# Kernel optimization log

Hardware: AMD Instinct MI355X
Metric: run time of the kernel (lower is better)

## Reference

```python
import jax, jax.numpy as jnp
import numpy as np

EPS = 1e-5  # torch BatchNorm2d default eps


def _conv(x, w, pad=0, groups=1):
    # x: NCHW, w: OIHW (torch layout); matches nn.Conv2d with given padding/groups
    return jax.lax.conv_general_dilated(
        x, w, window_strides=(1, 1), padding=[(pad, pad), (pad, pad)],
        dimension_numbers=("NCHW", "OIHW", "NCHW"), feature_group_count=groups)


def _bn_train(x, gamma, beta):
    # BatchNorm2d in training mode: batch stats over (N,H,W), biased variance
    m = jnp.mean(x, axis=(0, 2, 3), keepdims=True)
    v = jnp.mean(jnp.square(x - m), axis=(0, 2, 3), keepdims=True)
    return (x - m) * jax.lax.rsqrt(v + EPS) * gamma.reshape(1, -1, 1, 1) + beta.reshape(1, -1, 1, 1)


def setup_inputs() -> dict:
    key = jax.random.key(0)
    ks = jax.random.split(key, 8)
    B, C, H, W = 8, 32, 128, 128
    D = 8                      # num_directions
    WC = C * D                 # wavelet_channels = 256
    MID = WC * 2               # 512
    x = jax.random.normal(ks[0], (B, C, H, W), jnp.float32)
    # grouped directional filter bank: Conv2d(C, C*D, k=5, groups=C, bias=False)
    w_dir = jax.random.normal(ks[1], (WC, 1, 5, 5), jnp.float32) / np.sqrt(25.0)
    # wavelet_conv: Conv(WC->MID,3) BN ReLU Conv(MID->WC,3) BN ReLU
    w1 = jax.random.normal(ks[2], (MID, WC, 3, 3), jnp.float32) / np.sqrt(WC * 9.0)
    b1 = jnp.zeros((MID,), jnp.float32)
    g1 = jnp.ones((MID,), jnp.float32)
    be1 = jnp.zeros((MID,), jnp.float32)
    w2 = jax.random.normal(ks[3], (WC, MID, 3, 3), jnp.float32) / np.sqrt(MID * 9.0)
    b2 = jnp.zeros((WC,), jnp.float32)
    g2 = jnp.ones((WC,), jnp.float32)
    be2 = jnp.zeros((WC,), jnp.float32)
    # inverse_conv: Conv2d(WC, C, 1)
    w_inv = jax.random.normal(ks[4], (C, WC, 1, 1), jnp.float32) / np.sqrt(float(WC))
    b_inv = jnp.zeros((C,), jnp.float32)
    return {"x": x, "w_dir": w_dir, "w1": w1, "b1": b1, "g1": g1, "be1": be1,
            "w2": w2, "b2": b2, "g2": g2, "be2": be2, "w_inv": w_inv, "b_inv": b_inv}


def reference(x, w_dir, w1, b1, g1, be1, w2, b2, g2, be2, w_inv, b_inv):
    C = x.shape[1]
    # directional wavelet: grouped conv C -> C*8, k=5, pad=2, no bias
    coeffs = _conv(x, w_dir, pad=2, groups=C)                      # (B, 8C, H, W)
    # wavelet-domain conv stack
    h = _conv(coeffs, w1, pad=1) + b1.reshape(1, -1, 1, 1)         # (B, 16C, H, W)
    h = jax.nn.relu(_bn_train(h, g1, be1))
    h = _conv(h, w2, pad=1) + b2.reshape(1, -1, 1, 1)              # (B, 8C, H, W)
    h = jax.nn.relu(_bn_train(h, g2, be2))
    # inverse 1x1 conv back to C channels
    return _conv(h, w_inv) + b_inv.reshape(1, -1, 1, 1)            # (B, C, H, W)
```

## Files before the change

kernel.cpp:

```cpp
#include <hip/hip_runtime.h>

typedef unsigned short u16;
typedef unsigned int   u32;
typedef __attribute__((ext_vector_type(8)))  __bf16 bf16x8;
typedef __attribute__((ext_vector_type(4)))  float  f32x4;
typedef __attribute__((ext_vector_type(16))) float  f32x16;

__device__ __forceinline__ float bf2f(u16 u) {
    union { u32 i; float f; } v; v.i = ((u32)u) << 16; return v.f;
}
__device__ __forceinline__ u16 f2bf(float f) {
    u32 u = __float_as_uint(f);
    u32 r = (u + 0x7FFFu + ((u >> 16) & 1u)) >> 16;
    return (u16)r;
}

__device__ __forceinline__ void gl16(const u16* g, u16* l) {
    __builtin_amdgcn_global_load_lds(
        (const __attribute__((address_space(1))) unsigned int*)g,
        (__attribute__((address_space(3))) unsigned int*)l, 16, 0, 0);
}

__global__ __launch_bounds__(256) void dir_conv_k(const float* __restrict__ x,
                                                  const float* __restrict__ wd,
                                                  u16* __restrict__ coeffs) {
    int bid = blockIdx.x;
    int cc = bid & 3, y = (bid >> 2) & 127, n = bid >> 9;
    __shared__ float lx[5280];
    __shared__ float lw[1600];
    int t = threadIdx.x;
    for (int i = t; i < 1600; i += 256) {
        int ol = i / 25, tap = i - ol * 25;
        lw[tap * 64 + ol] = wd[(cc * 64 + ol) * 25 + tap];
    }
    for (int i = t; i < 5280; i += 256) {
        int c = i / 660, rem = i - c * 660;
        int ky = rem / 132, xx = rem - ky * 132;
        int gy = y - 2 + ky, gx = xx - 2;
        float v = 0.f;
        if (gy >= 0 && gy < 128 && gx >= 0 && gx < 128)
            v = x[(((n * 32 + cc * 8 + c) * 128 + gy) << 7) + gx];
        lx[i] = v;
    }
    __syncthreads();
    int px = t >> 1, oh = t & 1;
    float acc[4][8];
#pragma unroll
    for (int j = 0; j < 4; ++j)
#pragma unroll
        for (int d = 0; d < 8; ++d) acc[j][d] = 0.f;
#pragma unroll
    for (int j = 0; j < 4; ++j) {
        int cl = oh * 4 + j;
        const float* lxc = &lx[cl * 660];
#pragma unroll
        for (int ky = 0; ky < 5; ++ky)
#pragma unroll
            for (int kx = 0; kx < 5; ++kx) {
                float xv = lxc[ky * 132 + px + kx];
                const float* w8 = &lw[(ky * 5 + kx) * 64 + cl * 8];
#pragma unroll
                for (int d = 0; d < 8; ++d) acc[j][d] += xv * w8[d];
            }
    }
    long base = ((long)((n * 128 + y) * 128 + px)) * 256 + cc * 64 + oh * 32;
#pragma unroll
    for (int j = 0; j < 4; ++j) {
        uint4 o;
        o.x = (u32)f2bf(acc[j][0]) | ((u32)f2bf(acc[j][1]) << 16);
        o.y = (u32)f2bf(acc[j][2]) | ((u32)f2bf(acc[j][3]) << 16);
        o.z = (u32)f2bf(acc[j][4]) | ((u32)f2bf(acc[j][5]) << 16);
        o.w = (u32)f2bf(acc[j][6]) | ((u32)f2bf(acc[j][7]) << 16);
        *(uint4*)(coeffs + base + j * 8) = o;
    }
}

__global__ __launch_bounds__(256) void repack_w_k(const float* __restrict__ w,
                                                  u16* __restrict__ wp,
                                                  int OC, int IC, int total) {
    int f = blockIdx.x * 256 + threadIdx.x;
    if (f >= total) return;
    int KC = IC >> 5;
    int j  = f & 7;
    int h  = (f >> 3) & 1;
    int g  = f >> 4;
    int oc = g % OC; g /= OC;
    int s  = g & 1;  g >>= 1;
    int kc = g % KC;
    int tap = g / KC;
    int ic = kc * 32 + s * 16 + h * 8 + j;
    wp[f] = f2bf(w[(oc * IC + ic) * 9 + tap]);
}

#define KCITER(KCV, OFF)                                                       \
    {                                                                          \
        const int kc_ = (KCV);                                                 \
        const u16* lAu = (kc_ & 1) ? lA1 : lA0;                                \
        u16*       lAn = (kc_ & 1) ? lA0 : lA1;                                \
        __syncthreads();                                                       \
        {                                                                      \
            int au = ((h * 3) * W + lm) * 8;                                   \
            Ar[0][0] = *(const bf16x8*)(lAu + au);                             \
            Ar[0][1] = *(const bf16x8*)(lAu + au + 256);                       \
            Ar[0][2] = *(const bf16x8*)(lAu + au + 512);                       \
            Ar[0][3] = *(const bf16x8*)(lAu + au + 768);                       \
        }                                                                      \
        if (kc_ + 1 < KC) stage(lAn, kc_ + 1);                                 \
        _Pragma("unroll")                                                      \
        for (int i = 0; i < 18; ++i) {                                         \
            const int j   = (i + 1) % 18;                 \
            const int j3  = (i + 3) % 18;                \
            const int j3kc = (i >= 15) ? ((kc_ + 1 < KC) ? kc_ + 1 : 0) : kc_; \
            if (i != 17) {                                                     \
                const int jdy = j / 6, jdx = (j % 6) >> 1, js = j & 1;         \
                int au = (((js * 2 + h) * 3 + jdy) * W + jdx + lm) * 8;        \
                Ar[j & 1][0] = *(const bf16x8*)(lAu + au);                     \
                Ar[j & 1][1] = *(const bf16x8*)(lAu + au + 256);               \
                Ar[j & 1][2] = *(const bf16x8*)(lAu + au + 512);               \
                Ar[j & 1][3] = *(const bf16x8*)(lAu + au + 768);               \
            }                                                                  \
            bload(Br[(i + 3 + (OFF)) & 3], j3, j3kc);                          \
            __builtin_amdgcn_s_setprio(1);                                     \
            acc[0][0] = __builtin_amdgcn_mfma_f32_32x32x16_bf16(Ar[i & 1][0], Br[(i + (OFF)) & 3][0], acc[0][0], 0, 0, 0); \
            acc[0][1] = __builtin_amdgcn_mfma_f32_32x32x16_bf16(Ar[i & 1][0], Br[(i + (OFF)) & 3][1], acc[0][1], 0, 0, 0); \
            acc[1][0] = __builtin_amdgcn_mfma_f32_32x32x16_bf16(Ar[i & 1][1], Br[(i + (OFF)) & 3][0], acc[1][0], 0, 0, 0); \
            acc[1][1] = __builtin_amdgcn_mfma_f32_32x32x16_bf16(Ar[i & 1][1], Br[(i + (OFF)) & 3][1], acc[1][1], 0, 0, 0); \
            acc[2][0] = __builtin_amdgcn_mfma_f32_32x32x16_bf16(Ar[i & 1][2], Br[(i + (OFF)) & 3][0], acc[2][0], 0, 0, 0); \
            acc[2][1] = __builtin_amdgcn_mfma_f32_32x32x16_bf16(Ar[i & 1][2], Br[(i + (OFF)) & 3][1], acc[2][1], 0, 0, 0); \
            acc[3][0] = __builtin_amdgcn_mfma_f32_32x32x16_bf16(Ar[i & 1][3], Br[(i + (OFF)) & 3][0], acc[3][0], 0, 0, 0); \
            acc[3][1] = __builtin_amdgcn_mfma_f32_32x32x16_bf16(Ar[i & 1][3], Br[(i + (OFF)) & 3][1], acc[3][1], 0, 0, 0); \
            __builtin_amdgcn_s_setprio(0);                                     \
        }                                                                      \
    }

template<int IC, int OC>
__global__ __launch_bounds__(256, 2) void conv3_k(const u16* __restrict__ base,
                                                  u32 in_off,
                                                  const u16* __restrict__ wp,
                                                  const float* __restrict__ bias,
                                                  u32 zp_off,
                                                  u16* __restrict__ outp,
                                                  float* __restrict__ statp) {
    constexpr int KC = IC / 32;
    constexpr int W  = 130;
    constexpr int TU = 12 * W;
    constexpr int NFULL = TU / 256;
    constexpr int REM   = TU % 256;
    __shared__ u16 lA0[TU * 8];
    __shared__ u16 lA1[TU * 8];

    int bx0 = blockIdx.x;
    int bx = ((bx0 & 7) << 7) + (bx0 >> 3);
    int y = bx & 127, n = bx >> 7;
    int ocb = blockIdx.y;
    int t = threadIdx.x, lane = t & 63, wv = t >> 6;
    int lm = lane & 31, h = lane >> 5;
    int ocw = ocb * 256 + wv * 64;

    u32 off[NFULL + 1];
#pragma unroll
    for (int i = 0; i <= NFULL; ++i) {
        int u = (i == NFULL) ? (NFULL * 256 + lane) : (i * 256 + t);
        int icq = u / (3 * W);
        int r2  = u - icq * (3 * W);
        int dy  = r2 / W;
        int xx  = r2 - dy * W;
        int gy = y - 1 + dy, gx = xx - 1;
        bool ok = ((unsigned)gy < 128u) && ((unsigned)gx < 128u);
        off[i] = ok ? (in_off + (u32)((n * 128 + gy) * 128 + gx) * IC + (icq & 3) * 8)
                    : zp_off;
    }

    auto stage = [&](u16* dst, int kc) {
#pragma unroll
        for (int i = 0; i < NFULL; ++i)
            gl16(base + off[i] + kc * 32, dst + (i * 256 + wv * 64) * 8);
        if (wv == 0 && lane < REM)
            gl16(base + off[NFULL] + kc * 32, dst + NFULL * 256 * 8);
    };

    u32 wboff = (u32)(ocw + lm) * 16 + h * 8;
    bf16x8 Ar[2][4];
    bf16x8 Br[4][2];

    auto bload = [&](bf16x8* dst, int j, int kcv) {
        int jdy = j / 6, jdx = (j % 6) >> 1, js = j & 1;
        const u16* wb = wp + wboff
            + (u32)(((jdy * 3 + jdx) * KC + kcv) * 2 + js) * (OC * 16);
        dst[0] = *(const bf16x8*)wb;
        dst[1] = *(const bf16x8*)(wb + 512);
    };

    bload(Br[0], 0, 0);
    bload(Br[1], 1, 0);
    bload(Br[2], 2, 0);

    f32x16 acc[4][2];
#pragma unroll
    for (int mf = 0; mf < 4; ++mf)
#pragma unroll
        for (int nf = 0; nf < 2; ++nf)
#pragma unroll
            for (int r = 0; r < 16; ++r) acc[mf][nf][r] = 0.f;

    stage(lA0, 0);
    for (int kcb = 0; kcb < KC; kcb += 2) {
        KCITER(kcb, 0);
        KCITER(kcb + 1, 2);
    }

    long rowb = (long)(n * 128 + y) * 128;
    float ss[2] = {0.f, 0.f}, qq[2] = {0.f, 0.f};
#pragma unroll
    for (int nf = 0; nf < 2; ++nf) {
        int oc = ocw + nf * 32 + lm;
        float bi = bias[oc];
#pragma unroll
        for (int mf = 0; mf < 4; ++mf)
#pragma unroll
            for (int r = 0; r < 16; ++r) {
                int px = mf * 32 + (r & 3) + ((r >> 2) << 3) + (h << 2);
                u16 bv = f2bf(acc[mf][nf][r] + bi);
                outp[(rowb + px) * OC + oc] = bv;
                float vr = bf2f(bv);
                ss[nf] += vr;
                qq[nf] += vr * vr;
            }
    }
#pragma unroll
    for (int nf = 0; nf < 2; ++nf) {
        ss[nf] += __shfl_xor(ss[nf], 32);
        qq[nf] += __shfl_xor(qq[nf], 32);
    }
    if (h == 0) {
#pragma unroll
        for (int nf = 0; nf < 2; ++nf) {
            int oc = ocw + nf * 32 + lm;
            atomicAdd(&statp[oc * 2],     ss[nf]);
            atomicAdd(&statp[oc * 2 + 1], qq[nf]);
        }
    }
}

template<int C>
__global__ __launch_bounds__(256) void stats2_k(const float* __restrict__ part,
                                                const float* __restrict__ g,
                                                const float* __restrict__ be,
                                                float* __restrict__ ab) {
    int ch = blockIdx.x * 256 + threadIdx.x;
    if (ch >= C) return;
    float s = part[ch * 2], q = part[ch * 2 + 1];
    const float M = 131072.f;
    float mean = s / M;
    float var = q / M - mean * mean;
    float a = g[ch] * rsqrtf(var + 1e-5f);
    ab[ch * 2]     = a;
    ab[ch * 2 + 1] = be[ch] - mean * a;
}

__global__ __launch_bounds__(256) void bn_relu_k(u16* __restrict__ h,
                                                 const float* __restrict__ ab) {
    long idx8 = (long)blockIdx.x * 256 + threadIdx.x;
    u16* p = h + idx8 * 8;
    uint4 v = *(const uint4*)p;
    int chb = ((int)idx8 & 63) << 3;
    u32 w[4] = {v.x, v.y, v.z, v.w};
    u32 o[4];
#pragma unroll
    for (int q = 0; q < 4; ++q) {
        int ch = chb + q * 2;
        float2 a0 = *(const float2*)(ab + ch * 2);
        float2 a1 = *(const float2*)(ab + ch * 2 + 2);
        float f0 = bf2f((u16)(w[q] & 0xffff));
        float f1 = bf2f((u16)(w[q] >> 16));
        f0 = fmaxf(f0 * a0.x + a0.y, 0.f);
        f1 = fmaxf(f1 * a1.x + a1.y, 0.f);
        o[q] = (u32)f2bf(f0) | ((u32)f2bf(f1) << 16);
    }
    *(uint4*)p = make_uint4(o[0], o[1], o[2], o[3]);
}

__global__ __launch_bounds__(256) void inv_conv_k(const u16* __restrict__ h2,
                                                  const float* __restrict__ ab,
                                                  const float* __restrict__ winv,
                                                  const float* __restrict__ binv,
                                                  float* __restrict__ out) {
    __shared__ float lab[512];
    int t = threadIdx.x, lane = t & 63, wv = t >> 6;
    int lm = lane & 31, h = lane >> 5;
    lab[t] = ab[t];
    lab[t + 256] = ab[t + 256];
    __syncthreads();

    bf16x8 B[16];
#pragma unroll
    for (int s = 0; s < 16; ++s) {
        const float* wsrc = winv + lm * 256 + s * 16 + h * 8;
        union { bf16x8 v; u16 a[8]; } cv;
#pragma unroll
        for (int j = 0; j < 8; ++j) cv.a[j] = f2bf(wsrc[j]);
        B[s] = cv.v;
    }

    long pxw = (long)blockIdx.x * 256 + wv * 64;
    const u16* a0p = h2 + (pxw + lm) * 256 + h * 8;
    const u16* a1p = a0p + 32 * 256;

    f32x16 acc0, acc1;
#pragma unroll
    for (int r = 0; r < 16; ++r) { acc0[r] = 0.f; acc1[r] = 0.f; }

#pragma unroll
    for (int s = 0; s < 16; ++s) {
        int k0 = s * 16 + h * 8;
        uint4 v0 = *(const uint4*)(a0p + s * 16);
        uint4 v1 = *(const uint4*)(a1p + s * 16);
        u32 w0[4] = {v0.x, v0.y, v0.z, v0.w};
        u32 w1[4] = {v1.x, v1.y, v1.z, v1.w};
        union { bf16x8 v; u16 a[8]; } A0, A1;
#pragma unroll
        for (int j = 0; j < 8; ++j) {
            float aab = lab[(k0 + j) * 2], bbb = lab[(k0 + j) * 2 + 1];
            u16 u0 = (j & 1) ? (u16)(w0[j >> 1] >> 16) : (u16)(w0[j >> 1] & 0xffff);
            u16 u1 = (j & 1) ? (u16)(w1[j >> 1] >> 16) : (u16)(w1[j >> 1] & 0xffff);
            A0.a[j] = f2bf(fmaxf(bf2f(u0) * aab + bbb, 0.f));
            A1.a[j] = f2bf(fmaxf(bf2f(u1) * aab + bbb, 0.f));
        }
        acc0 = __builtin_amdgcn_mfma_f32_32x32x16_bf16(A0.v, B[s], acc0, 0, 0, 0);
        acc1 = __builtin_amdgcn_mfma_f32_32x32x16_bf16(A1.v, B[s], acc1, 0, 0, 0);
    }

    float bi = binv[lm];
    int n = (int)(pxw >> 14);
    int prem = (int)(pxw & 16383);
    float* ob = out + (((long)(n * 32 + lm)) << 14) + prem + 4 * h;
#pragma unroll
    for (int g = 0; g < 4; ++g) {
        f32x4 o0, o1;
#pragma unroll
        for (int i = 0; i < 4; ++i) { o0[i] = acc0[g * 4 + i] + bi; o1[i] = acc1[g * 4 + i] + bi; }
        *(f32x4*)(ob + g * 8)      = o0;
        *(f32x4*)(ob + 32 + g * 8) = o1;
    }
}

extern "C" void kernel_launch(void* const* d_in, const int* in_sizes, int n_in,
                              void* d_out, int out_size, void* d_ws, size_t ws_size,
                              hipStream_t stream) {
    const float* x     = (const float*)d_in[0];
    const float* w_dir = (const float*)d_in[1];
    const float* w1    = (const float*)d_in[2];
    const float* b1    = (const float*)d_in[3];
    const float* g1    = (const float*)d_in[4];
    const float* be1   = (const float*)d_in[5];
    const float* w2    = (const float*)d_in[6];
    const float* b2    = (const float*)d_in[7];
    const float* g2    = (const float*)d_in[8];
    const float* be2   = (const float*)d_in[9];
    const float* w_inv = (const float*)d_in[10];
    const float* b_inv = (const float*)d_in[11];
    float* out = (float*)d_out;
    char* ws = (char*)d_ws;

    u16*   w1p   = (u16*)(ws + 0);
    u16*   w2p   = (u16*)(ws + 2359296);
    float* part1 = (float*)(ws + 4718592);
    float* part2 = (float*)(ws + 4722688);
    float* ab1   = (float*)(ws + 5242880);
    float* ab2   = (float*)(ws + 5246976);
    u16*   zp    = (u16*)(ws + 5249024);
    u16*   coef  = (u16*)(ws + 8388608);
    u16*   h1    = (u16*)(ws + 75497472);
    const u16* basep = (const u16*)ws;
    u32 zp_off   = 5249024 / 2;
    u32 coef_off = 8388608 / 2;
    u32 h1_off   = 75497472 / 2;

    hipMemsetAsync(zp, 0, 1024, stream);
    hipMemsetAsync(part1, 0, 8192, stream);
    repack_w_k<<<4608, 256, 0, stream>>>(w1, w1p, 512, 256, 1179648);
    repack_w_k<<<4608, 256, 0, stream>>>(w2, w2p, 256, 512, 1179648);
    dir_conv_k<<<4096, 256, 0, stream>>>(x, w_dir, coef);
    conv3_k<256, 512><<<dim3(1024, 2), 256, 0, stream>>>(basep, coef_off, w1p, b1, zp_off, h1, part1);
    stats2_k<512><<<2, 256, 0, stream>>>(part1, g1, be1, ab1);
    bn_relu_k<<<32768, 256, 0, stream>>>(h1, ab1);
    conv3_k<512, 256><<<dim3(1024, 1), 256, 0, stream>>>(basep, h1_off, w2p, b2, zp_off, coef, part2);
    stats2_k<256><<<1, 256, 0, stream>>>(part2, g2, be2, ab2);
    inv_conv_k<<<512, 256, 0, stream>>>(coef, ab2, w_inv, b_inv, out);
}
```

Before: 694.7 us.

## Switch conv3 MFMA from 32x32x16 to 16x16x32 with matching weight layout

Reworks the implicit-GEMM 3x3 conv kernel to use 16x16x32 bf16 MFMA instead of 32x32x16, giving each wave an 8x4 grid of 16x16 tiles. The inner loop now covers 9 taps with a full 32-wide K per step instead of 18 half-steps. The weight repack layout, LDS A-fragment reads, B-fragment loads and epilogue indexing and stat reductions all change to match. It trades fewer, longer MFMA issues for more, shorter ones and twice as many A registers, which raises register pressure.

Result: no change. 702.1 us (+1.1%).

```diff
diff --git a/kernel.cpp b/kernel.cpp
--- a/kernel.cpp
+++ b/kernel.cpp
@@ -81,16 +81,34 @@
     int f = blockIdx.x * 256 + threadIdx.x;
     if (f >= total) return;
     int KC = IC >> 5;
-    int j  = f & 7;
-    int h  = (f >> 3) & 1;
-    int g  = f >> 4;
-    int oc = g % OC; g /= OC;
-    int s  = g & 1;  g >>= 1;
+    int OG = OC >> 4;
+    int j = f & 7;
+    int l = (f >> 3) & 63;
+    int g = f >> 9;
+    int ocg = g % OG; g /= OG;
     int kc = g % KC;
     int tap = g / KC;
-    int ic = kc * 32 + s * 16 + h * 8 + j;
+    int oc = ocg * 16 + (l & 15);
+    int ic = kc * 32 + (l >> 4) * 8 + j;
     wp[f] = f2bf(w[(oc * IC + ic) * 9 + tap]);
 }
+
+#define AREAD(P, lAu, DY, DX)                                                  \
+    {                                                                          \
+        int au_ = ((kq * 3 + (DY)) * W + (DX) + l15) * 8;                      \
+        _Pragma("unroll")                                                      \
+        for (int mf_ = 0; mf_ < 8; ++mf_)                                      \
+            Ar[P][mf_] = *(const bf16x8*)((lAu) + au_ + mf_ * 128);            \
+    }
+
+#define MFMA32(P)                                                              \
+    _Pragma("unroll")                                                          \
+    for (int mf_ = 0; mf_ < 8; ++mf_) {                                        \
+        acc[mf_][0] = __builtin_amdgcn_mfma_f32_16x16x32_bf16(Ar[P][mf_], Br[P][0], acc[mf_][0], 0, 0, 0); \
+        acc[mf_][1] = __builtin_amdgcn_mfma_f32_16x16x32_bf16(Ar[P][mf_], Br[P][1], acc[mf_][1], 0, 0, 0); \
+        acc[mf_][2] = __builtin_amdgcn_mfma_f32_16x16x32_bf16(Ar[P][mf_], Br[P][2], acc[mf_][2], 0, 0, 0); \
+        acc[mf_][3] = __builtin_amdgcn_mfma_f32_16x16x32_bf16(Ar[P][mf_], Br[P][3], acc[mf_][3], 0, 0, 0); \
+    }
 
 #define KCITER(KCV, OFF)                                                       \
     {                                                                          \
@@ -98,37 +116,16 @@
         const u16* lAu = (kc_ & 1) ? lA1 : lA0;                                \
         u16*       lAn = (kc_ & 1) ? lA0 : lA1;                                \
         __syncthreads();                                                       \
-        {                                                                      \
-            int au = ((h * 3) * W + lm) * 8;                                   \
-            Ar[0][0] = *(const bf16x8*)(lAu + au);                             \
-            Ar[0][1] = *(const bf16x8*)(lAu + au + 256);                       \
-            Ar[0][2] = *(const bf16x8*)(lAu + au + 512);                       \
-            Ar[0][3] = *(const bf16x8*)(lAu + au + 768);                       \
-        }                                                                      \
+        AREAD((OFF), lAu, 0, 0);                                               \
         if (kc_ + 1 < KC) stage(lAn, kc_ + 1);                                 \
         _Pragma("unroll")                                                      \
-        for (int i = 0; i < 18; ++i) {                                         \
-            const int j   = (i + 1) % 18;                 \
-            const int j3  = (i + 3) % 18;                \
-            const int j3kc = (i >= 15) ? ((kc_ + 1 < KC) ? kc_ + 1 : 0) : kc_; \
-            if (i != 17) {                                                     \
-                const int jdy = j / 6, jdx = (j % 6) >> 1, js = j & 1;         \
-                int au = (((js * 2 + h) * 3 + jdy) * W + jdx + lm) * 8;        \
-                Ar[j & 1][0] = *(const bf16x8*)(lAu + au);                     \
-                Ar[j & 1][1] = *(const bf16x8*)(lAu + au + 256);               \
-                Ar[j & 1][2] = *(const bf16x8*)(lAu + au + 512);               \
-                Ar[j & 1][3] = *(const bf16x8*)(lAu + au + 768);               \
-            }                                                                  \
-            bload(Br[(i + 3 + (OFF)) & 3], j3, j3kc);                          \
+        for (int i = 0; i < 9; ++i) {                                          \
+            const int jt = (i + 1) % 9;                                        \
+            const int jkc = (i == 8) ? ((kc_ + 1 < KC) ? kc_ + 1 : 0) : kc_;   \
+            if (i != 8) AREAD(((i + 1 + (OFF)) & 1), lAu, (jt / 3), (jt % 3)); \
+            bload(Br[(i + 1 + (OFF)) & 1], jt, jkc);                           \
             __builtin_amdgcn_s_setprio(1);                                     \
-            acc[0][0] = __builtin_amdgcn_mfma_f32_32x32x16_bf16(Ar[i & 1][0], Br[(i + (OFF)) & 3][0], acc[0][0], 0, 0, 0); \
-            acc[0][1] = __builtin_amdgcn_mfma_f32_32x32x16_bf16(Ar[i & 1][0], Br[(i + (OFF)) & 3][1], acc[0][1], 0, 0, 0); \
-            acc[1][0] = __builtin_amdgcn_mfma_f32_32x32x16_bf16(Ar[i & 1][1], Br[(i + (OFF)) & 3][0], acc[1][0], 0, 0, 0); \
-            acc[1][1] = __builtin_amdgcn_mfma_f32_32x32x16_bf16(Ar[i & 1][1], Br[(i + (OFF)) & 3][1], acc[1][1], 0, 0, 0); \
-            acc[2][0] = __builtin_amdgcn_mfma_f32_32x32x16_bf16(Ar[i & 1][2], Br[(i + (OFF)) & 3][0], acc[2][0], 0, 0, 0); \
-            acc[2][1] = __builtin_amdgcn_mfma_f32_32x32x16_bf16(Ar[i & 1][2], Br[(i + (OFF)) & 3][1], acc[2][1], 0, 0, 0); \
-            acc[3][0] = __builtin_amdgcn_mfma_f32_32x32x16_bf16(Ar[i & 1][3], Br[(i + (OFF)) & 3][0], acc[3][0], 0, 0, 0); \
-            acc[3][1] = __builtin_amdgcn_mfma_f32_32x32x16_bf16(Ar[i & 1][3], Br[(i + (OFF)) & 3][1], acc[3][1], 0, 0, 0); \
+            MFMA32(((i + (OFF)) & 1));                                         \
             __builtin_amdgcn_s_setprio(0);                                     \
         }                                                                      \
     }
@@ -154,7 +151,7 @@
     int y = bx & 127, n = bx >> 7;
     int ocb = blockIdx.y;
     int t = threadIdx.x, lane = t & 63, wv = t >> 6;
-    int lm = lane & 31, h = lane >> 5;
+    int l15 = lane & 15, kq = lane >> 4;
     int ocw = ocb * 256 + wv * 64;
 
     u32 off[NFULL + 1];
@@ -179,47 +176,45 @@
             gl16(base + off[NFULL] + kc * 32, dst + NFULL * 256 * 8);
     };
 
-    u32 wboff = (u32)(ocw + lm) * 16 + h * 8;
-    bf16x8 Ar[2][4];
-    bf16x8 Br[4][2];
-
-    auto bload = [&](bf16x8* dst, int j, int kcv) {
-        int jdy = j / 6, jdx = (j % 6) >> 1, js = j & 1;
-        const u16* wb = wp + wboff
-            + (u32)(((jdy * 3 + jdx) * KC + kcv) * 2 + js) * (OC * 16);
+    u32 wboff = (u32)(ocw >> 4) * 512 + (u32)lane * 8;
+    bf16x8 Ar[2][8];
+    bf16x8 Br[2][4];
+
+    auto bload = [&](bf16x8* dst, int jt, int kcv) {
+        const u16* wb = wp + (u32)((jt * KC + kcv) * (OC >> 4)) * 512 + wboff;
         dst[0] = *(const bf16x8*)wb;
         dst[1] = *(const bf16x8*)(wb + 512);
+        dst[2] = *(const bf16x8*)(wb + 1024);
+        dst[3] = *(const bf16x8*)(wb + 1536);
     };
 
     bload(Br[0], 0, 0);
-    bload(Br[1], 1, 0);
-    bload(Br[2], 2, 0);
-
-    f32x16 acc[4][2];
-#pragma unroll
-    for (int mf = 0; mf < 4; ++mf)
-#pragma unroll
-        for (int nf = 0; nf < 2; ++nf)
-#pragma unroll
-            for (int r = 0; r < 16; ++r) acc[mf][nf][r] = 0.f;
+
+    f32x4 acc[8][4];
+#pragma unroll
+    for (int mf = 0; mf < 8; ++mf)
+#pragma unroll
+        for (int nf = 0; nf < 4; ++nf)
+#pragma unroll
+            for (int r = 0; r < 4; ++r) acc[mf][nf][r] = 0.f;
 
     stage(lA0, 0);
     for (int kcb = 0; kcb < KC; kcb += 2) {
         KCITER(kcb, 0);
-        KCITER(kcb + 1, 2);
+        KCITER(kcb + 1, 1);
     }
 
     long rowb = (long)(n * 128 + y) * 128;
-    float ss[2] = {0.f, 0.f}, qq[2] = {0.f, 0.f};
-#pragma unroll
-    for (int nf = 0; nf < 2; ++nf) {
-        int oc = ocw + nf * 32 + lm;
+    float ss[4] = {0.f, 0.f, 0.f, 0.f}, qq[4] = {0.f, 0.f, 0.f, 0.f};
+#pragma unroll
+    for (int nf = 0; nf < 4; ++nf) {
+        int oc = ocw + nf * 16 + l15;
         float bi = bias[oc];
 #pragma unroll
-        for (int mf = 0; mf < 4; ++mf)
-#pragma unroll
-            for (int r = 0; r < 16; ++r) {
-                int px = mf * 32 + (r & 3) + ((r >> 2) << 3) + (h << 2);
+        for (int mf = 0; mf < 8; ++mf)
+#pragma unroll
+            for (int r = 0; r < 4; ++r) {
+                int px = mf * 16 + kq * 4 + r;
                 u16 bv = f2bf(acc[mf][nf][r] + bi);
                 outp[(rowb + px) * OC + oc] = bv;
                 float vr = bf2f(bv);
@@ -228,14 +223,16 @@
             }
     }
 #pragma unroll
-    for (int nf = 0; nf < 2; ++nf) {
+    for (int nf = 0; nf < 4; ++nf) {
+        ss[nf] += __shfl_xor(ss[nf], 16);
         ss[nf] += __shfl_xor(ss[nf], 32);
+        qq[nf] += __shfl_xor(qq[nf], 16);
         qq[nf] += __shfl_xor(qq[nf], 32);
     }
-    if (h == 0) {
-#pragma unroll
-        for (int nf = 0; nf < 2; ++nf) {
-            int oc = ocw + nf * 32 + lm;
+    if (lane < 16) {
+#pragma unroll
+        for (int nf = 0; nf < 4; ++nf) {
+            int oc = ocw + nf * 16 + lane;
             atomicAdd(&statp[oc * 2],     ss[nf]);
             atomicAdd(&statp[oc * 2 + 1], qq[nf]);
         }
```
